# Optimization experiments

Measured on AMD Instinct MI355X. Metric: run time of the kernel, lower is better.

## Reference

```python
import jax, jax.numpy as jnp
import numpy as np

B, S, D, H = 2, 2048, 1024, 16
DK = D // H
NEG = -1e9


def setup_inputs() -> dict:
    key = jax.random.key(0)
    ks = jax.random.split(key, 12)
    sc = 1.0 / np.sqrt(D)
    inp = {
        "query": jax.random.normal(ks[0], (B, S, D), jnp.float32),
        "key": jax.random.normal(ks[1], (B, S, D), jnp.float32),
        "value": jax.random.normal(ks[2], (B, S, D), jnp.float32),
        "mask": jnp.ones((B, 1, S), jnp.int32),
        "Wq": jax.random.normal(ks[3], (D, D), jnp.float32) * sc,
        "bq": jnp.zeros((D,), jnp.float32),
        "Wk": jax.random.normal(ks[4], (D, D), jnp.float32) * sc,
        "bk": jnp.zeros((D,), jnp.float32),
        "Wv": jax.random.normal(ks[5], (D, D), jnp.float32) * sc,
        "bv": jnp.zeros((D,), jnp.float32),
        "Wo": jax.random.normal(ks[6], (D, D), jnp.float32) * sc,
        "bo": jnp.zeros((D,), jnp.float32),
    }
    return inp


def reference(query, key, value, mask, Wq, bq, Wk, bk, Wv, bv, Wo, bo):
    # projections + split heads: [B,S,D] -> [B,H,S,DK]
    def proj(x, W, b):
        return (x @ W + b).reshape(B, S, H, DK).transpose(0, 2, 1, 3)

    q = proj(query, Wq, bq)
    k = proj(key, Wk, bk)
    v = proj(value, Wv, bv)

    scores = jnp.einsum("bhqd,bhkd->bhqk", q, k) / jnp.sqrt(jnp.float32(DK))
    # mask: [B,1,S] -> unsqueeze head dim -> [B,1,1,S], broadcast over heads & queries
    m = mask[:, None, :, :]  # [B,1,1,S]
    scores = jnp.where(m == 0, NEG, scores)
    p_attn = jax.nn.softmax(scores, axis=-1)  # dropout p=0 (eval)
    x = jnp.einsum("bhqk,bhkd->bhqd", p_attn, v)
    x = x.transpose(0, 2, 1, 3).reshape(B, S, D)
    return x @ Wo + bo
```

## Files before the change

kernel.cpp:

```cpp
#include <hip/hip_runtime.h>
#include <stdint.h>

typedef unsigned short u16;
typedef __bf16 bf16x8 __attribute__((ext_vector_type(8), may_alias));
typedef unsigned short u16x8 __attribute__((ext_vector_type(8), may_alias));
typedef unsigned short u16x4 __attribute__((ext_vector_type(4), may_alias));
typedef float f32x4 __attribute__((ext_vector_type(4)));
typedef float f32x16 __attribute__((ext_vector_type(16)));
typedef int i32x2 __attribute__((ext_vector_type(2)));

__device__ __forceinline__ u16 f2bf(float f) {
    union { float f; uint32_t i; } v; v.f = f;
    return (u16)((v.i + 0x7FFFu + ((v.i >> 16) & 1u)) >> 16);
}

__device__ __forceinline__ float exp2_hw(float x) {
#if __has_builtin(__builtin_amdgcn_exp2f)
    return __builtin_amdgcn_exp2f(x);
#else
    float r; asm("v_exp_f32 %0, %1" : "=v"(r) : "v"(x)); return r;
#endif
}

__device__ __forceinline__ uint32_t cvt_pk_bf16(float a, float b) {
    uint32_t r;
    asm("v_cvt_pk_bf16_f32 %0, %1, %2" : "=v"(r) : "v"(a), "v"(b));
    return r;
}

__device__ __forceinline__ void pl32swap(uint32_t& a, uint32_t& b) {
#if __has_builtin(__builtin_amdgcn_permlane32_swap)
    i32x2 r = __builtin_amdgcn_permlane32_swap((int)a, (int)b, false, false);
    a = (uint32_t)r[0]; b = (uint32_t)r[1];
#else
    asm("v_permlane32_swap_b32 %0, %1" : "+v"(a), "+v"(b));
#endif
}

__device__ __forceinline__ void gld_lds16(const u16* g, u16* l) {
    __builtin_amdgcn_global_load_lds(
        (const __attribute__((address_space(1))) unsigned int*)g,
        (__attribute__((address_space(3))) unsigned int*)l, 16, 0, 0);
}

__global__ __launch_bounds__(256) void cvt_all(
    const float* __restrict__ s0, const float* __restrict__ s1, const float* __restrict__ s2,
    const float* __restrict__ w0, const float* __restrict__ w1,
    const float* __restrict__ w2, const float* __restrict__ w3,
    u16* __restrict__ d0, u16* __restrict__ d1, u16* __restrict__ d2,
    u16* __restrict__ t0, u16* __restrict__ t1,
    u16* __restrict__ t2, u16* __restrict__ t3)
{
    __shared__ float L[64][65];
    const int z = blockIdx.z;
    const int tid = threadIdx.x;
    if (z < 3) {
        const float* s = (z == 0) ? s0 : (z == 1) ? s1 : s2;
        u16*         d = (z == 0) ? d0 : (z == 1) ? d1 : d2;
        const size_t base = ((size_t)blockIdx.x * 256 + tid) * 16;
        #pragma unroll
        for (int p = 0; p < 2; ++p) {
            float4 a = *reinterpret_cast<const float4*>(s + base + p * 8);
            float4 b = *reinterpret_cast<const float4*>(s + base + p * 8 + 4);
            u16x8 o;
            o[0] = f2bf(a.x); o[1] = f2bf(a.y); o[2] = f2bf(a.z); o[3] = f2bf(a.w);
            o[4] = f2bf(b.x); o[5] = f2bf(b.y); o[6] = f2bf(b.z); o[7] = f2bf(b.w);
            *reinterpret_cast<u16x8*>(d + base + p * 8) = o;
        }
    } else {
        if (blockIdx.x >= 256) return;
        const int zi = z - 3;
        const float* w = (zi == 0) ? w0 : (zi == 1) ? w1 : (zi == 2) ? w2 : w3;
        u16*         t = (zi == 0) ? t0 : (zi == 1) ? t1 : (zi == 2) ? t2 : t3;
        const int k0 = (blockIdx.x & 15) * 64, n0 = (blockIdx.x >> 4) * 64;
        const int rr = tid >> 6, cc = tid & 63;
        #pragma unroll
        for (int p = 0; p < 16; ++p)
            L[p * 4 + rr][cc] = w[(size_t)(k0 + p * 4 + rr) * 1024 + n0 + cc];
        __syncthreads();
        #pragma unroll
        for (int p = 0; p < 16; ++p)
            t[(size_t)(n0 + p * 4 + rr) * 1024 + k0 + cc] = f2bf(L[cc][p * 4 + rr]);
    }
}

__global__ __launch_bounds__(256) void gemm_bt(
    const u16* __restrict__ A0, const u16* __restrict__ A1, const u16* __restrict__ A2,
    const u16* __restrict__ B0, const u16* __restrict__ B1, const u16* __restrict__ B2,
    const float* __restrict__ c0, const float* __restrict__ c1, const float* __restrict__ c2,
    void* __restrict__ d0, void* __restrict__ d1, void* __restrict__ d2,
    int mode_override)
{
    __shared__ u16 As[2 * 4096];
    __shared__ u16 Bs[2 * 4096];

    const int z = blockIdx.z;
    const u16* A = (z == 0) ? A0 : (z == 1) ? A1 : A2;
    const u16* BT = (z == 0) ? B0 : (z == 1) ? B1 : B2;
    const float* bias = (z == 0) ? c0 : (z == 1) ? c1 : c2;
    void* dst = (z == 0) ? d0 : (z == 1) ? d1 : d2;
    const int mode = (mode_override >= 0) ? mode_override : ((z == 2) ? 2 : 0);

    const int tid  = threadIdx.x;
    const int wave = tid >> 6, lane = tid & 63;
    const int quad = lane >> 4, l15 = lane & 15;
    const int row0 = blockIdx.x * 128, col0 = blockIdx.y * 128;
    const int wrow = (wave >> 1) * 64, wcol = (wave & 1) * 64;

    const int sidx0 = tid, sidx1 = 256 + tid;
    const int sr0 = sidx0 >> 2, sc0 = ((sidx0 & 3) ^ ((sr0 >> 1) & 3)) * 8;
    const int sr1 = sidx1 >> 2, sc1 = ((sidx1 & 3) ^ ((sr1 >> 1) & 3)) * 8;
    const size_t aoff0 = (size_t)(row0 + sr0) * 1024 + sc0;
    const size_t aoff1 = (size_t)(row0 + sr1) * 1024 + sc1;
    const size_t boff0 = (size_t)(col0 + sr0) * 1024 + sc0;
    const size_t boff1 = (size_t)(col0 + sr1) * 1024 + sc1;
    u16* const asl0 = &As[(size_t)(wave * 64) * 8];
    u16* const asl1 = &As[(size_t)(256 + wave * 64) * 8];
    u16* const bsl0 = &Bs[(size_t)(wave * 64) * 8];
    u16* const bsl1 = &Bs[(size_t)(256 + wave * 64) * 8];

    f32x4 acc[4][4] = {};

    gld_lds16(A + aoff0, asl0);
    gld_lds16(BT + boff0, bsl0);
    gld_lds16(A + aoff1, asl1);
    gld_lds16(BT + boff1, bsl1);
    __syncthreads();

    int cur = 0;
    for (int k0 = 0; k0 < 1024; k0 += 32) {
        if (k0 < 992) {
            const int nb = (cur ^ 1) * 4096;
            gld_lds16(A + aoff0 + (k0 + 32), asl0 + nb);
            gld_lds16(BT + boff0 + (k0 + 32), bsl0 + nb);
            gld_lds16(A + aoff1 + (k0 + 32), asl1 + nb);
            gld_lds16(BT + boff1 + (k0 + 32), bsl1 + nb);
        }

        const u16* Ab = &As[cur * 4096];
        const u16* Bb = &Bs[cur * 4096];
        bf16x8 a[4], b[4];
        #pragma unroll
        for (int i = 0; i < 4; ++i) {
            const int ar = wrow + i * 16 + l15;
            a[i] = *reinterpret_cast<const bf16x8*>(&Ab[ar * 32 + (quad ^ ((ar >> 1) & 3)) * 8]);
        }
        #pragma unroll
        for (int j = 0; j < 4; ++j) {
            const int br = wcol + j * 16 + l15;
            b[j] = *reinterpret_cast<const bf16x8*>(&Bb[br * 32 + (quad ^ ((br >> 1) & 3)) * 8]);
        }
        #pragma unroll
        for (int i = 0; i < 4; ++i)
            #pragma unroll
            for (int j = 0; j < 4; ++j)
                acc[i][j] = __builtin_amdgcn_mfma_f32_16x16x32_bf16(a[i], b[j], acc[i][j], 0, 0, 0);

        __syncthreads();
        cur ^= 1;
    }

    const float emul = (mode == 0 && z == 0 && mode_override < 0) ? 0.18033688011112042f : 1.0f;

    #pragma unroll
    for (int i = 0; i < 4; ++i) {
        #pragma unroll
        for (int j = 0; j < 4; ++j) {
            const int gc  = col0 + wcol + j * 16 + l15;
            const float bv = bias[gc];
            const int gr0 = row0 + wrow + i * 16 + quad * 4;
            if (mode == 3) {
                float* df = (float*)dst;
                #pragma unroll
                for (int r = 0; r < 4; ++r)
                    df[(size_t)(gr0 + r) * 1024 + gc] = acc[i][j][r] + bv;
            } else if (mode == 2) {
                u16* dp = (u16*)dst;
                const int b = gr0 >> 11, s = gr0 & 2047;
                const int h = gc >> 6,  dk = gc & 63;
                u16x4 pk;
                pk[0] = f2bf(acc[i][j][0] + bv);
                pk[1] = f2bf(acc[i][j][1] + bv);
                pk[2] = f2bf(acc[i][j][2] + bv);
                pk[3] = f2bf(acc[i][j][3] + bv);
                *reinterpret_cast<u16x4*>(dp + ((size_t)((b * 16 + h) * 64 + dk)) * 2048 + s) = pk;
            } else {
                u16* dp = (u16*)dst;
                #pragma unroll
                for (int r = 0; r < 4; ++r) {
                    const int gr = gr0 + r;
                    const int b = gr >> 11, s = gr & 2047;
                    const int h = gc >> 6, dk = gc & 63;
                    dp[((size_t)((b * 16 + h) * 2048 + s)) * 64 + dk] = f2bf((acc[i][j][r] + bv) * emul);
                }
            }
        }
    }
}

__global__ __launch_bounds__(512, 4) void attn_fused(
    const u16* __restrict__ Qb, const u16* __restrict__ Kb,
    const u16* __restrict__ Vt, const int* __restrict__ mask,
    u16* __restrict__ ctx)
{
    __shared__ __align__(16) u16 SMEM[16896];

    const int tid  = threadIdx.x;
    const int w    = tid >> 6;
    const int lane = tid & 63;
    const int l31  = lane & 31;
    const int hi   = lane >> 5;
    const int qw   = w & 3;
    const int kh   = w >> 2;

    const int id = blockIdx.x;
    const int sw = (id & 7) * 64 + (id >> 3);
    const int bh = sw >> 4;
    const int q0 = (sw & 15) * 128;
    const int b  = bh >> 4, h = bh & 15;

    const u16* Qp = Qb + (size_t)bh * 2048 * 64;
    const u16* Kp = Kb + (size_t)bh * 2048 * 64;
    const u16* Vp = Vt + (size_t)bh * 64 * 2048;
    const int* mp = mask + b * 2048;

    bf16x8 qf[4];
    {
        const u16* qrow = Qp + (size_t)(q0 + qw * 32 + l31) * 64 + hi * 8;
        #pragma unroll
        for (int s = 0; s < 4; ++s)
            qf[s] = *reinterpret_cast<const bf16x8*>(qrow + s * 16);
    }

    const u16* kgs = Kp + (size_t)(lane ^ w) * 64 + w * 8;
    const u16* vgs = Vp + (size_t)(lane ^ w) * 2048 + w * 8;

    gld_lds16(kgs, &SMEM[w * 512]);
    gld_lds16(vgs, &SMEM[4096 + w * 512]);
    int mreg = mp[lane];
    __syncthreads();

    f32x16 accO0 = {}, accO1 = {};
    float la0 = 0.f, la1 = 0.f, la2 = 0.f, la3 = 0.f;

    int cur = 0;
    for (int t = 0; t < 32; ++t) {
        const int kk = t * 64;
        int mnext = 1;
        if (t < 31) {
            const int nb = (cur ^ 1) * 8192;
            gld_lds16(kgs + (size_t)(kk + 64) * 64, &SMEM[nb + w * 512]);
            gld_lds16(vgs + (kk + 64), &SMEM[nb + 4096 + w * 512]);
            mnext = mp[kk + 64 + lane];
        }
        const u16* Kb_ = &SMEM[cur * 8192];
        const u16* Vb_ = &SMEM[cur * 8192 + 4096];

        const bool fullmask = (__ballot(mreg != 0) == ~0ull);

        f32x16 z = {};
        __builtin_amdgcn_s_setprio(1);
        #pragma unroll
        for (int s = 0; s < 4; ++s) {
            const int cb = s * 2 + hi;
            const bf16x8 ak = *reinterpret_cast<const bf16x8*>(
                &Kb_[cb * 512 + (((kh * 32 + l31)) ^ cb) * 8]);
            z = __builtin_amdgcn_mfma_f32_32x32x16_bf16(ak, qf[s], z, 0, 0, 0);
        }
        __builtin_amdgcn_s_setprio(0);
        float p[16];
        #pragma unroll
        for (int r = 0; r < 16; ++r) p[r] = exp2_hw(z[r]);
        if (!fullmask) {
            #pragma unroll
            for (int r = 0; r < 16; ++r) {
                const int kv = kk + kh * 32 + (r & 3) + 8 * (r >> 2) + 4 * hi;
                if (mp[kv] == 0) p[r] = 0.f;
            }
        }
        la0 += p[0] + p[4] + p[8]  + p[12];
        la1 += p[1] + p[5] + p[9]  + p[13];
        la2 += p[2] + p[6] + p[10] + p[14];
        la3 += p[3] + p[7] + p[11] + p[15];

        uint32_t wd0 = cvt_pk_bf16(p[0],  p[1]);
        uint32_t wd1 = cvt_pk_bf16(p[2],  p[3]);
        uint32_t wd2 = cvt_pk_bf16(p[4],  p[5]);
        uint32_t wd3 = cvt_pk_bf16(p[6],  p[7]);
        uint32_t wd4 = cvt_pk_bf16(p[8],  p[9]);
        uint32_t wd5 = cvt_pk_bf16(p[10], p[11]);
        uint32_t wd6 = cvt_pk_bf16(p[12], p[13]);
        uint32_t wd7 = cvt_pk_bf16(p[14], p[15]);
        pl32swap(wd0, wd2);
        pl32swap(wd1, wd3);
        pl32swap(wd4, wd6);
        pl32swap(wd5, wd7);
        union { uint32_t u[4]; bf16x8 v; } A0, A1;
        A0.u[0] = wd0; A0.u[1] = wd1; A0.u[2] = wd2; A0.u[3] = wd3;
        A1.u[0] = wd4; A1.u[1] = wd5; A1.u[2] = wd6; A1.u[3] = wd7;

        const int ck0 = kh * 4 + hi;
        const int ck1 = kh * 4 + 2 + hi;
        const bf16x8 bv00 = *reinterpret_cast<const bf16x8*>(&Vb_[ck0 * 512 + ((     l31) ^ ck0) * 8]);
        const bf16x8 bv01 = *reinterpret_cast<const bf16x8*>(&Vb_[ck1 * 512 + ((     l31) ^ ck1) * 8]);
        const bf16x8 bv10 = *reinterpret_cast<const bf16x8*>(&Vb_[ck0 * 512 + ((32 + l31) ^ ck0) * 8]);
        const bf16x8 bv11 = *reinterpret_cast<const bf16x8*>(&Vb_[ck1 * 512 + ((32 + l31) ^ ck1) * 8]);
        __builtin_amdgcn_s_setprio(1);
        accO0 = __builtin_amdgcn_mfma_f32_32x32x16_bf16(A0.v, bv00, accO0, 0, 0, 0);
        accO0 = __builtin_amdgcn_mfma_f32_32x32x16_bf16(A1.v, bv01, accO0, 0, 0, 0);
        accO1 = __builtin_amdgcn_mfma_f32_32x32x16_bf16(A0.v, bv10, accO1, 0, 0, 0);
        accO1 = __builtin_amdgcn_mfma_f32_32x32x16_bf16(A1.v, bv11, accO1, 0, 0, 0);
        __builtin_amdgcn_s_setprio(0);

        __syncthreads();
        cur ^= 1;
        mreg = mnext;
    }

    float l_part = (la0 + la1) + (la2 + la3);
    l_part += __shfl_xor(l_part, 32);
    float* F = (float*)SMEM;
    if (kh) {
        #pragma unroll
        for (int r = 0; r < 16; ++r) F[qw * 1024 + r * 64 + lane] = accO0[r];
        #pragma unroll
        for (int r = 0; r < 16; ++r) F[4096 + qw * 1024 + r * 64 + lane] = accO1[r];
        if (lane < 32) F[8192 + qw * 32 + l31] = l_part;
    }
    __syncthreads();
    if (!kh && lane < 32)
        F[8320 + qw * 32 + l31] = 1.0f / (l_part + F[8192 + qw * 32 + l31]);
    __syncthreads();
    if (!kh) {
        #pragma unroll
        for (int r = 0; r < 16; ++r) {
            const int qr = (r & 3) + 8 * (r >> 2) + 4 * hi;
            const float iv = F[8320 + qw * 32 + qr];
            const float o0 = accO0[r] + F[qw * 1024 + r * 64 + lane];
            const float o1 = accO1[r] + F[4096 + qw * 1024 + r * 64 + lane];
            u16* row = ctx + (size_t)(b * 2048 + q0 + qw * 32 + qr) * 1024 + h * 64;
            row[l31]      = f2bf(o0 * iv);
            row[32 + l31] = f2bf(o1 * iv);
        }
    }
}

extern "C" void kernel_launch(void* const* d_in, const int* in_sizes, int n_in,
                              void* d_out, int out_size, void* d_ws, size_t ws_size,
                              hipStream_t stream) {
    const float* query = (const float*)d_in[0];
    const float* key   = (const float*)d_in[1];
    const float* value = (const float*)d_in[2];
    const int*   mask  = (const int*)d_in[3];
    const float* Wq = (const float*)d_in[4];
    const float* bq = (const float*)d_in[5];
    const float* Wk = (const float*)d_in[6];
    const float* bk = (const float*)d_in[7];
    const float* Wv = (const float*)d_in[8];
    const float* bv = (const float*)d_in[9];
    const float* Wo = (const float*)d_in[10];
    const float* bo = (const float*)d_in[11];
    float* out = (float*)d_out;

    u16* ws   = (u16*)d_ws;
    u16* Xq   = ws;
    u16* Xk   = ws + 4194304;
    u16* Xv   = ws + 8388608;
    u16* WqT  = ws + 12582912;
    u16* WkT  = ws + 13631488;
    u16* WvT  = ws + 14680064;
    u16* WoT  = ws + 15728640;
    u16* Qb   = ws + 16777216;
    u16* Kb   = ws + 20971520;
    u16* Vt   = ws + 25165824;
    u16* ctx  = Xq;

    dim3 blk(256);
    cvt_all<<<dim3(1024, 1, 7), blk, 0, stream>>>(query, key, value, Wq, Wk, Wv, Wo,
                                                  Xq, Xk, Xv, WqT, WkT, WvT, WoT);
    gemm_bt<<<dim3(32, 8, 3),  blk, 0, stream>>>(Xq, Xk, Xv, WqT, WkT, WvT,
                                                 bq, bk, bv, Qb, Kb, Vt, -1);
    attn_fused<<<dim3(512), dim3(512), 0, stream>>>(Qb, Kb, Vt, mask, ctx);
    gemm_bt<<<dim3(32, 8, 1),  blk, 0, stream>>>(ctx, ctx, ctx, WoT, WoT, WoT,
                                                 bo, bo, bo, out, out, out, 3);
}
```

Baseline: 226.0 us.

## Load K and V fragments directly from global into registers, dropping LDS staging

Replaces the double-buffered global-to-LDS staging of K and V tiles with direct per-lane global loads into MFMA operand registers. K fragments for the next tile are prefetched in registers during the current iteration, and the per-iteration block barrier is removed. This cuts LDS traffic and synchronisation. The cost is redundant global/L2 reads across the four query waves that share each K/V tile, and exposed global latency for V, which is loaded in the same iteration it is used.

```diff
diff --git a/kernel.cpp b/kernel.cpp
--- a/kernel.cpp
+++ b/kernel.cpp
@@ -203,7 +203,7 @@
     const u16* __restrict__ Vt, const int* __restrict__ mask,
     u16* __restrict__ ctx)
 {
-    __shared__ __align__(16) u16 SMEM[16896];
+    __shared__ __align__(16) float F[8448];
 
     const int tid  = threadIdx.x;
     const int w    = tid >> 6;
@@ -232,42 +232,40 @@
             qf[s] = *reinterpret_cast<const bf16x8*>(qrow + s * 16);
     }
 
-    const u16* kgs = Kp + (size_t)(lane ^ w) * 64 + w * 8;
-    const u16* vgs = Vp + (size_t)(lane ^ w) * 2048 + w * 8;
-
-    gld_lds16(kgs, &SMEM[w * 512]);
-    gld_lds16(vgs, &SMEM[4096 + w * 512]);
+    const u16* KA  = Kp + (size_t)(kh * 32 + l31) * 64 + hi * 8;
+    const u16* VA0 = Vp + (size_t)l31 * 2048 + kh * 32 + hi * 8;
+    const u16* VA1 = VA0 + 32 * 2048;
+
+    bf16x8 ka0 = *reinterpret_cast<const bf16x8*>(KA);
+    bf16x8 ka1 = *reinterpret_cast<const bf16x8*>(KA + 16);
+    bf16x8 ka2 = *reinterpret_cast<const bf16x8*>(KA + 32);
+    bf16x8 ka3 = *reinterpret_cast<const bf16x8*>(KA + 48);
     int mreg = mp[lane];
-    __syncthreads();
 
     f32x16 accO0 = {}, accO1 = {};
     float la0 = 0.f, la1 = 0.f, la2 = 0.f, la3 = 0.f;
 
-    int cur = 0;
     for (int t = 0; t < 32; ++t) {
         const int kk = t * 64;
+        const u16* vb0 = VA0 + kk;
+        const u16* vb1 = VA1 + kk;
+        const bf16x8 v00 = *reinterpret_cast<const bf16x8*>(vb0);
+        const bf16x8 v01 = *reinterpret_cast<const bf16x8*>(vb0 + 16);
+        const bf16x8 v10 = *reinterpret_cast<const bf16x8*>(vb1);
+        const bf16x8 v11 = *reinterpret_cast<const bf16x8*>(vb1 + 16);
         int mnext = 1;
-        if (t < 31) {
-            const int nb = (cur ^ 1) * 8192;
-            gld_lds16(kgs + (size_t)(kk + 64) * 64, &SMEM[nb + w * 512]);
-            gld_lds16(vgs + (kk + 64), &SMEM[nb + 4096 + w * 512]);
-            mnext = mp[kk + 64 + lane];
-        }
-        const u16* Kb_ = &SMEM[cur * 8192];
-        const u16* Vb_ = &SMEM[cur * 8192 + 4096];
+        if (t < 31) mnext = mp[kk + 64 + lane];
 
         const bool fullmask = (__ballot(mreg != 0) == ~0ull);
 
         f32x16 z = {};
         __builtin_amdgcn_s_setprio(1);
-        #pragma unroll
-        for (int s = 0; s < 4; ++s) {
-            const int cb = s * 2 + hi;
-            const bf16x8 ak = *reinterpret_cast<const bf16x8*>(
-                &Kb_[cb * 512 + (((kh * 32 + l31)) ^ cb) * 8]);
-            z = __builtin_amdgcn_mfma_f32_32x32x16_bf16(ak, qf[s], z, 0, 0, 0);
-        }
+        z = __builtin_amdgcn_mfma_f32_32x32x16_bf16(ka0, qf[0], z, 0, 0, 0);
+        z = __builtin_amdgcn_mfma_f32_32x32x16_bf16(ka1, qf[1], z, 0, 0, 0);
+        z = __builtin_amdgcn_mfma_f32_32x32x16_bf16(ka2, qf[2], z, 0, 0, 0);
+        z = __builtin_amdgcn_mfma_f32_32x32x16_bf16(ka3, qf[3], z, 0, 0, 0);
         __builtin_amdgcn_s_setprio(0);
+
         float p[16];
         #pragma unroll
         for (int r = 0; r < 16; ++r) p[r] = exp2_hw(z[r]);
@@ -299,27 +297,26 @@
         A0.u[0] = wd0; A0.u[1] = wd1; A0.u[2] = wd2; A0.u[3] = wd3;
         A1.u[0] = wd4; A1.u[1] = wd5; A1.u[2] = wd6; A1.u[3] = wd7;
 
-        const int ck0 = kh * 4 + hi;
-        const int ck1 = kh * 4 + 2 + hi;
-        const bf16x8 bv00 = *reinterpret_cast<const bf16x8*>(&Vb_[ck0 * 512 + ((     l31) ^ ck0) * 8]);
-        const bf16x8 bv01 = *reinterpret_cast<const bf16x8*>(&Vb_[ck1 * 512 + ((     l31) ^ ck1) * 8]);
-        const bf16x8 bv10 = *reinterpret_cast<const bf16x8*>(&Vb_[ck0 * 512 + ((32 + l31) ^ ck0) * 8]);
-        const bf16x8 bv11 = *reinterpret_cast<const bf16x8*>(&Vb_[ck1 * 512 + ((32 + l31) ^ ck1) * 8]);
+        {
+            const u16* kn = KA + (size_t)((t < 31) ? (t + 1) : t) * 4096;
+            ka0 = *reinterpret_cast<const bf16x8*>(kn);
+            ka1 = *reinterpret_cast<const bf16x8*>(kn + 16);
+            ka2 = *reinterpret_cast<const bf16x8*>(kn + 32);
+            ka3 = *reinterpret_cast<const bf16x8*>(kn + 48);
+        }
+
         __builtin_amdgcn_s_setprio(1);
-        accO0 = __builtin_amdgcn_mfma_f32_32x32x16_bf16(A0.v, bv00, accO0, 0, 0, 0);
-        accO0 = __builtin_amdgcn_mfma_f32_32x32x16_bf16(A1.v, bv01, accO0, 0, 0, 0);
-        accO1 = __builtin_amdgcn_mfma_f32_32x32x16_bf16(A0.v, bv10, accO1, 0, 0, 0);
-        accO1 = __builtin_amdgcn_mfma_f32_32x32x16_bf16(A1.v, bv11, accO1, 0, 0, 0);
+        accO0 = __builtin_amdgcn_mfma_f32_32x32x16_bf16(A0.v, v00, accO0, 0, 0, 0);
+        accO0 = __builtin_amdgcn_mfma_f32_32x32x16_bf16(A1.v, v01, accO0, 0, 0, 0);
+        accO1 = __builtin_amdgcn_mfma_f32_32x32x16_bf16(A0.v, v10, accO1, 0, 0, 0);
+        accO1 = __builtin_amdgcn_mfma_f32_32x32x16_bf16(A1.v, v11, accO1, 0, 0, 0);
         __builtin_amdgcn_s_setprio(0);
 
-        __syncthreads();
-        cur ^= 1;
         mreg = mnext;
     }
 
     float l_part = (la0 + la1) + (la2 + la3);
     l_part += __shfl_xor(l_part, 32);
-    float* F = (float*)SMEM;
     if (kh) {
         #pragma unroll
         for (int r = 0; r < 16; ++r) F[qw * 1024 + r * 64 + lane] = accO0[r];
```

Measured after the change: 300.5 us. 1.33x slower.

## Fuse fp32-to-bf16 activation conversion into projection GEMM and compute softmax sum via MFMA

Applied to the files above, without the earlier changes.

Removes the separate conversion pass over query/key/value and instead loads fp32 activations inside the projection GEMM. There they are converted to bf16 in registers and stored to LDS after the MFMAs, overlapping the conversion with compute. In the attention kernel, the per-tile mask ballot is replaced by a one-time all-ones check, and the row-sum of probabilities is accumulated with extra MFMAs against a ones vector instead of scalar adds. This saves a full read/write of the activations but doubles the A-operand global traffic in the GEMM and adds register pressure and extra MFMA work.

```diff
diff --git a/kernel.cpp b/kernel.cpp
--- a/kernel.cpp
+++ b/kernel.cpp
@@ -43,59 +43,40 @@
         (__attribute__((address_space(3))) unsigned int*)l, 16, 0, 0);
 }
 
-__global__ __launch_bounds__(256) void cvt_all(
-    const float* __restrict__ s0, const float* __restrict__ s1, const float* __restrict__ s2,
+__global__ __launch_bounds__(256) void cvt_w(
     const float* __restrict__ w0, const float* __restrict__ w1,
     const float* __restrict__ w2, const float* __restrict__ w3,
-    u16* __restrict__ d0, u16* __restrict__ d1, u16* __restrict__ d2,
     u16* __restrict__ t0, u16* __restrict__ t1,
     u16* __restrict__ t2, u16* __restrict__ t3)
 {
     __shared__ float L[64][65];
-    const int z = blockIdx.z;
+    const int zi = blockIdx.z;
     const int tid = threadIdx.x;
-    if (z < 3) {
-        const float* s = (z == 0) ? s0 : (z == 1) ? s1 : s2;
-        u16*         d = (z == 0) ? d0 : (z == 1) ? d1 : d2;
-        const size_t base = ((size_t)blockIdx.x * 256 + tid) * 16;
-        #pragma unroll
-        for (int p = 0; p < 2; ++p) {
-            float4 a = *reinterpret_cast<const float4*>(s + base + p * 8);
-            float4 b = *reinterpret_cast<const float4*>(s + base + p * 8 + 4);
-            u16x8 o;
-            o[0] = f2bf(a.x); o[1] = f2bf(a.y); o[2] = f2bf(a.z); o[3] = f2bf(a.w);
-            o[4] = f2bf(b.x); o[5] = f2bf(b.y); o[6] = f2bf(b.z); o[7] = f2bf(b.w);
-            *reinterpret_cast<u16x8*>(d + base + p * 8) = o;
-        }
-    } else {
-        if (blockIdx.x >= 256) return;
-        const int zi = z - 3;
-        const float* w = (zi == 0) ? w0 : (zi == 1) ? w1 : (zi == 2) ? w2 : w3;
-        u16*         t = (zi == 0) ? t0 : (zi == 1) ? t1 : (zi == 2) ? t2 : t3;
-        const int k0 = (blockIdx.x & 15) * 64, n0 = (blockIdx.x >> 4) * 64;
-        const int rr = tid >> 6, cc = tid & 63;
-        #pragma unroll
-        for (int p = 0; p < 16; ++p)
-            L[p * 4 + rr][cc] = w[(size_t)(k0 + p * 4 + rr) * 1024 + n0 + cc];
-        __syncthreads();
-        #pragma unroll
-        for (int p = 0; p < 16; ++p)
-            t[(size_t)(n0 + p * 4 + rr) * 1024 + k0 + cc] = f2bf(L[cc][p * 4 + rr]);
-    }
+    const float* w = (zi == 0) ? w0 : (zi == 1) ? w1 : (zi == 2) ? w2 : w3;
+    u16*         t = (zi == 0) ? t0 : (zi == 1) ? t1 : (zi == 2) ? t2 : t3;
+    const int k0 = (blockIdx.x & 15) * 64, n0 = (blockIdx.x >> 4) * 64;
+    const int rr = tid >> 6, cc = tid & 63;
+    #pragma unroll
+    for (int p = 0; p < 16; ++p)
+        L[p * 4 + rr][cc] = w[(size_t)(k0 + p * 4 + rr) * 1024 + n0 + cc];
+    __syncthreads();
+    #pragma unroll
+    for (int p = 0; p < 16; ++p)
+        t[(size_t)(n0 + p * 4 + rr) * 1024 + k0 + cc] = f2bf(L[cc][p * 4 + rr]);
 }
 
 __global__ __launch_bounds__(256) void gemm_bt(
-    const u16* __restrict__ A0, const u16* __restrict__ A1, const u16* __restrict__ A2,
+    const void* __restrict__ A0v, const void* __restrict__ A1v, const void* __restrict__ A2v,
     const u16* __restrict__ B0, const u16* __restrict__ B1, const u16* __restrict__ B2,
     const float* __restrict__ c0, const float* __restrict__ c1, const float* __restrict__ c2,
     void* __restrict__ d0, void* __restrict__ d1, void* __restrict__ d2,
-    int mode_override)
+    int mode_override, int a_f32)
 {
     __shared__ u16 As[2 * 4096];
     __shared__ u16 Bs[2 * 4096];
 
     const int z = blockIdx.z;
-    const u16* A = (z == 0) ? A0 : (z == 1) ? A1 : A2;
+    const void* Av = (z == 0) ? A0v : (z == 1) ? A1v : A2v;
     const u16* BT = (z == 0) ? B0 : (z == 1) ? B1 : B2;
     const float* bias = (z == 0) ? c0 : (z == 1) ? c1 : c2;
     void* dst = (z == 0) ? d0 : (z == 1) ? d1 : d2;
@@ -119,21 +100,47 @@
     u16* const bsl0 = &Bs[(size_t)(wave * 64) * 8];
     u16* const bsl1 = &Bs[(size_t)(256 + wave * 64) * 8];
 
+    const u16*   A16 = (const u16*)Av;
+    const float* A32 = (const float*)Av;
+
     f32x4 acc[4][4] = {};
 
-    gld_lds16(A + aoff0, asl0);
+    if (a_f32) {
+        float4 x00 = *reinterpret_cast<const float4*>(A32 + aoff0);
+        float4 x01 = *reinterpret_cast<const float4*>(A32 + aoff0 + 4);
+        float4 x10 = *reinterpret_cast<const float4*>(A32 + aoff1);
+        float4 x11 = *reinterpret_cast<const float4*>(A32 + aoff1 + 4);
+        union { uint32_t u[4]; u16x8 v; } P0, P1;
+        P0.u[0] = cvt_pk_bf16(x00.x, x00.y); P0.u[1] = cvt_pk_bf16(x00.z, x00.w);
+        P0.u[2] = cvt_pk_bf16(x01.x, x01.y); P0.u[3] = cvt_pk_bf16(x01.z, x01.w);
+        P1.u[0] = cvt_pk_bf16(x10.x, x10.y); P1.u[1] = cvt_pk_bf16(x10.z, x10.w);
+        P1.u[2] = cvt_pk_bf16(x11.x, x11.y); P1.u[3] = cvt_pk_bf16(x11.z, x11.w);
+        *reinterpret_cast<u16x8*>(&As[(size_t)sidx0 * 8]) = P0.v;
+        *reinterpret_cast<u16x8*>(&As[(size_t)sidx1 * 8]) = P1.v;
+    } else {
+        gld_lds16(A16 + aoff0, asl0);
+        gld_lds16(A16 + aoff1, asl1);
+    }
     gld_lds16(BT + boff0, bsl0);
-    gld_lds16(A + aoff1, asl1);
     gld_lds16(BT + boff1, bsl1);
     __syncthreads();
 
     int cur = 0;
     for (int k0 = 0; k0 < 1024; k0 += 32) {
-        if (k0 < 992) {
+        const bool pref = (k0 < 992);
+        float4 n00, n01, n10, n11;
+        if (pref) {
             const int nb = (cur ^ 1) * 4096;
-            gld_lds16(A + aoff0 + (k0 + 32), asl0 + nb);
+            if (a_f32) {
+                n00 = *reinterpret_cast<const float4*>(A32 + aoff0 + (k0 + 32));
+                n01 = *reinterpret_cast<const float4*>(A32 + aoff0 + (k0 + 32) + 4);
+                n10 = *reinterpret_cast<const float4*>(A32 + aoff1 + (k0 + 32));
+                n11 = *reinterpret_cast<const float4*>(A32 + aoff1 + (k0 + 32) + 4);
+            } else {
+                gld_lds16(A16 + aoff0 + (k0 + 32), asl0 + nb);
+                gld_lds16(A16 + aoff1 + (k0 + 32), asl1 + nb);
+            }
             gld_lds16(BT + boff0 + (k0 + 32), bsl0 + nb);
-            gld_lds16(A + aoff1 + (k0 + 32), asl1 + nb);
             gld_lds16(BT + boff1 + (k0 + 32), bsl1 + nb);
         }
 
@@ -155,6 +162,17 @@
             #pragma unroll
             for (int j = 0; j < 4; ++j)
                 acc[i][j] = __builtin_amdgcn_mfma_f32_16x16x32_bf16(a[i], b[j], acc[i][j], 0, 0, 0);
+
+        if (pref && a_f32) {
+            const int nb = (cur ^ 1) * 4096;
+            union { uint32_t u[4]; u16x8 v; } P0, P1;
+            P0.u[0] = cvt_pk_bf16(n00.x, n00.y); P0.u[1] = cvt_pk_bf16(n00.z, n00.w);
+            P0.u[2] = cvt_pk_bf16(n01.x, n01.y); P0.u[3] = cvt_pk_bf16(n01.z, n01.w);
+            P1.u[0] = cvt_pk_bf16(n10.x, n10.y); P1.u[1] = cvt_pk_bf16(n10.z, n10.w);
+            P1.u[2] = cvt_pk_bf16(n11.x, n11.y); P1.u[3] = cvt_pk_bf16(n11.z, n11.w);
+            *reinterpret_cast<u16x8*>(&As[nb + (size_t)sidx0 * 8]) = P0.v;
+            *reinterpret_cast<u16x8*>(&As[nb + (size_t)sidx1 * 8]) = P1.v;
+        }
 
         __syncthreads();
         cur ^= 1;
@@ -237,26 +255,30 @@
 
     gld_lds16(kgs, &SMEM[w * 512]);
     gld_lds16(vgs, &SMEM[4096 + w * 512]);
-    int mreg = mp[lane];
+
+    int allone = 1;
+    #pragma unroll 1
+    for (int t = 0; t < 32; ++t) {
+        const int m = mp[t * 64 + lane];
+        allone &= (__ballot(m != 0) == ~0ull) ? 1 : 0;
+    }
     __syncthreads();
 
-    f32x16 accO0 = {}, accO1 = {};
-    float la0 = 0.f, la1 = 0.f, la2 = 0.f, la3 = 0.f;
+    union { uint32_t u[4]; bf16x8 v; } ON;
+    ON.u[0] = ON.u[1] = ON.u[2] = ON.u[3] = 0x3F803F80u;
+
+    f32x16 accO0 = {}, accO1 = {}, accL = {};
 
     int cur = 0;
     for (int t = 0; t < 32; ++t) {
         const int kk = t * 64;
-        int mnext = 1;
         if (t < 31) {
             const int nb = (cur ^ 1) * 8192;
             gld_lds16(kgs + (size_t)(kk + 64) * 64, &SMEM[nb + w * 512]);
             gld_lds16(vgs + (kk + 64), &SMEM[nb + 4096 + w * 512]);
-            mnext = mp[kk + 64 + lane];
         }
         const u16* Kb_ = &SMEM[cur * 8192];
         const u16* Vb_ = &SMEM[cur * 8192 + 4096];
-
-        const bool fullmask = (__ballot(mreg != 0) == ~0ull);
 
         f32x16 z = {};
         __builtin_amdgcn_s_setprio(1);
@@ -268,20 +290,17 @@
             z = __builtin_amdgcn_mfma_f32_32x32x16_bf16(ak, qf[s], z, 0, 0, 0);
         }
         __builtin_amdgcn_s_setprio(0);
+
         float p[16];
         #pragma unroll
         for (int r = 0; r < 16; ++r) p[r] = exp2_hw(z[r]);
-        if (!fullmask) {
+        if (!allone) {
             #pragma unroll
             for (int r = 0; r < 16; ++r) {
                 const int kv = kk + kh * 32 + (r & 3) + 8 * (r >> 2) + 4 * hi;
                 if (mp[kv] == 0) p[r] = 0.f;
             }
         }
-        la0 += p[0] + p[4] + p[8]  + p[12];
-        la1 += p[1] + p[5] + p[9]  + p[13];
-        la2 += p[2] + p[6] + p[10] + p[14];
-        la3 += p[3] + p[7] + p[11] + p[15];
 
         uint32_t wd0 = cvt_pk_bf16(p[0],  p[1]);
         uint32_t wd1 = cvt_pk_bf16(p[2],  p[3]);
@@ -310,32 +329,34 @@
         accO0 = __builtin_amdgcn_mfma_f32_32x32x16_bf16(A1.v, bv01, accO0, 0, 0, 0);
         accO1 = __builtin_amdgcn_mfma_f32_32x32x16_bf16(A0.v, bv10, accO1, 0, 0, 0);
         accO1 = __builtin_amdgcn_mfma_f32_32x32x16_bf16(A1.v, bv11, accO1, 0, 0, 0);
+        accL  = __builtin_amdgcn_mfma_f32_32x32x16_bf16(A0.v, ON.v, accL, 0, 0, 0);
+        accL  = __builtin_amdgcn_mfma_f32_32x32x16_bf16(A1.v, ON.v, accL, 0, 0, 0);
         __builtin_amdgcn_s_setprio(0);
 
         __syncthreads();
         cur ^= 1;
-        mreg = mnext;
-    }
-
-    float l_part = (la0 + la1) + (la2 + la3);
-    l_part += __shfl_xor(l_part, 32);
+    }
+
     float* F = (float*)SMEM;
     if (kh) {
         #pragma unroll
         for (int r = 0; r < 16; ++r) F[qw * 1024 + r * 64 + lane] = accO0[r];
         #pragma unroll
         for (int r = 0; r < 16; ++r) F[4096 + qw * 1024 + r * 64 + lane] = accO1[r];
-        if (lane < 32) F[8192 + qw * 32 + l31] = l_part;
-    }
-    __syncthreads();
-    if (!kh && lane < 32)
-        F[8320 + qw * 32 + l31] = 1.0f / (l_part + F[8192 + qw * 32 + l31]);
+        if (l31 == 0) {
+            #pragma unroll
+            for (int r = 0; r < 16; ++r) {
+                const int qr = (r & 3) + 8 * (r >> 2) + 4 * hi;
+                F[8192 + qw * 32 + qr] = accL[r];
+            }
+        }
+    }
     __syncthreads();
     if (!kh) {
         #pragma unroll
         for (int r = 0; r < 16; ++r) {
             const int qr = (r & 3) + 8 * (r >> 2) + 4 * hi;
-            const float iv = F[8320 + qw * 32 + qr];
+            const float iv = 1.0f / (accL[r] + F[8192 + qw * 32 + qr]);
             const float o0 = accO0[r] + F[qw * 1024 + r * 64 + lane];
             const float o1 = accO1[r] + F[4096 + qw * 1024 + r * 64 + lane];
             u16* row = ctx + (size_t)(b * 2048 + q0 + qw * 32 + qr) * 1024 + h * 64;
@@ -363,9 +384,7 @@
     float* out = (float*)d_out;
 
     u16* ws   = (u16*)d_ws;
-    u16* Xq   = ws;
-    u16* Xk   = ws + 4194304;
-    u16* Xv   = ws + 8388608;
+    u16* ctx  = ws;
     u16* WqT  = ws + 12582912;
     u16* WkT  = ws + 13631488;
     u16* WvT  = ws + 14680064;
@@ -373,14 +392,15 @@
     u16* Qb   = ws + 16777216;
     u16* Kb   = ws + 20971520;
     u16* Vt   = ws + 25165824;
-    u16* ctx  = Xq;
 
     dim3 blk(256);
-    cvt_all<<<dim3(1024, 1, 7), blk, 0, stream>>>(query, key, value, Wq, Wk, Wv, Wo,
-                                                  Xq, Xk, Xv, WqT, WkT, WvT, WoT);
-    gemm_bt<<<dim3(32, 8, 3),  blk, 0, stream>>>(Xq, Xk, Xv, WqT, WkT, WvT,
-                                                 bq, bk, bv, Qb, Kb, Vt, -1);
+    cvt_w<<<dim3(256, 1, 4), blk, 0, stream>>>(Wq, Wk, Wv, Wo,
+                                               WqT, WkT, WvT, WoT);
+    gemm_bt<<<dim3(32, 8, 3), blk, 0, stream>>>(query, key, value,
+                                                WqT, WkT, WvT,
+                                                bq, bk, bv, Qb, Kb, Vt, -1, 1);
     attn_fused<<<dim3(512), dim3(512), 0, stream>>>(Qb, Kb, Vt, mask, ctx);
-    gemm_bt<<<dim3(32, 8, 1),  blk, 0, stream>>>(ctx, ctx, ctx, WoT, WoT, WoT,
-                                                 bo, bo, bo, out, out, out, 3);
-}
+    gemm_bt<<<dim3(32, 8, 1), blk, 0, stream>>>(ctx, ctx, ctx,
+                                                WoT, WoT, WoT,
+                                                bo, bo, bo, out, out, out, 3, 0);
+}
```

Result: slower. 270.1 us (+19.5%).

## Triple-buffer GEMM LDS tiles with two-ahead prefetch and partial vmcnt waits

Applied to the files above, without the earlier changes.

Changes the projection GEMM's shared-memory staging from double to triple buffering. Global-to-LDS loads are issued two K-steps ahead, and a partial s_waitcnt vmcnt(4) replaces __syncthreads, so one tile's loads stay in flight across the barrier. This aims to hide more global memory latency behind the MFMA work. In exchange LDS use grows by half, which can reduce occupancy, and correctness now depends on the hand-written waitcnt counts matching the load issue order.

```diff
diff --git a/kernel.cpp b/kernel.cpp
--- a/kernel.cpp
+++ b/kernel.cpp
@@ -91,8 +91,8 @@
     void* __restrict__ d0, void* __restrict__ d1, void* __restrict__ d2,
     int mode_override)
 {
-    __shared__ u16 As[2 * 4096];
-    __shared__ u16 Bs[2 * 4096];
+    __shared__ u16 As[3 * 4096];
+    __shared__ u16 Bs[3 * 4096];
 
     const int z = blockIdx.z;
     const u16* A = (z == 0) ? A0 : (z == 1) ? A1 : A2;
@@ -121,24 +121,33 @@
 
     f32x4 acc[4][4] = {};
 
-    gld_lds16(A + aoff0, asl0);
-    gld_lds16(BT + boff0, bsl0);
-    gld_lds16(A + aoff1, asl1);
-    gld_lds16(BT + boff1, bsl1);
-    __syncthreads();
-
-    int cur = 0;
-    for (int k0 = 0; k0 < 1024; k0 += 32) {
-        if (k0 < 992) {
-            const int nb = (cur ^ 1) * 4096;
-            gld_lds16(A + aoff0 + (k0 + 32), asl0 + nb);
-            gld_lds16(BT + boff0 + (k0 + 32), bsl0 + nb);
-            gld_lds16(A + aoff1 + (k0 + 32), asl1 + nb);
-            gld_lds16(BT + boff1 + (k0 + 32), bsl1 + nb);
-        }
-
-        const u16* Ab = &As[cur * 4096];
-        const u16* Bb = &Bs[cur * 4096];
+    {
+        gld_lds16(A + aoff0, asl0);
+        gld_lds16(BT + boff0, bsl0);
+        gld_lds16(A + aoff1, asl1);
+        gld_lds16(BT + boff1, bsl1);
+        gld_lds16(A + aoff0 + 32, asl0 + 4096);
+        gld_lds16(BT + boff0 + 32, bsl0 + 4096);
+        gld_lds16(A + aoff1 + 32, asl1 + 4096);
+        gld_lds16(BT + boff1 + 32, bsl1 + 4096);
+    }
+    asm volatile("s_waitcnt vmcnt(4)" ::: "memory");
+    __builtin_amdgcn_s_barrier();
+    __builtin_amdgcn_sched_barrier(0);
+
+    for (int t = 0; t < 32; ++t) {
+        const int rd = t % 3;
+        if (t < 30) {
+            const int nb = ((t + 2) % 3) * 4096;
+            const int kc = (t + 2) * 32;
+            gld_lds16(A + aoff0 + kc, asl0 + nb);
+            gld_lds16(BT + boff0 + kc, bsl0 + nb);
+            gld_lds16(A + aoff1 + kc, asl1 + nb);
+            gld_lds16(BT + boff1 + kc, bsl1 + nb);
+        }
+
+        const u16* Ab = &As[rd * 4096];
+        const u16* Bb = &Bs[rd * 4096];
         bf16x8 a[4], b[4];
         #pragma unroll
         for (int i = 0; i < 4; ++i) {
@@ -156,8 +165,10 @@
             for (int j = 0; j < 4; ++j)
                 acc[i][j] = __builtin_amdgcn_mfma_f32_16x16x32_bf16(a[i], b[j], acc[i][j], 0, 0, 0);
 
-        __syncthreads();
-        cur ^= 1;
+        if (t < 30) asm volatile("s_waitcnt vmcnt(4)" ::: "memory");
+        else        asm volatile("s_waitcnt vmcnt(0)" ::: "memory");
+        __builtin_amdgcn_s_barrier();
+        __builtin_amdgcn_sched_barrier(0);
     }
 
     const float emul = (mode == 0 && z == 0 && mode_override < 0) ? 0.18033688011112042f : 1.0f;
```

Result: slower. 237.1 us (+4.9%).
